# Optimization experiments

Measured on AMD Instinct MI355X. Metric: run time of the kernel, lower is better.

The kernel has to match this reference:

```python
import jax, jax.numpy as jnp
import numpy as np

L = 8          # num_layers
H = 1024       # hidden_size
F = 4096       # features_per_layer
B, S = 2, 1024 # batch, seq_len
P = L * (L + 1) // 2  # number of (layer -> target_layer) decoders


def setup_inputs() -> dict:
    key = jax.random.key(0)
    k0, k1, k2, k3 = jax.random.split(key, 4)
    res = jax.random.normal(k0, (L, B, S, H), jnp.float32)          # residual stream per layer
    We = jax.random.normal(k1, (L, F, H), jnp.float32) / np.sqrt(H)  # stacked encoder weights
    be = jnp.zeros((L, F), jnp.float32)
    Wd = jax.random.normal(k2, (P, H, F), jnp.float32) / np.sqrt(F)  # flattened decoder weights, pair (l,t>=l)
    bd = jnp.zeros((P, H), jnp.float32)
    thresh = jnp.full((L,), 0.03, jnp.float32)                       # JumpReLU thresholds
    return {"res": res, "We": We, "be": be, "Wd": Wd, "bd": bd, "thresh": thresh}


def reference(res, We, be, Wd, bd, thresh):
    # Encoders + JumpReLU (eval-mode: x * (x > threshold)) for all layers at once
    preact = jnp.einsum('lbsh,lfh->lbsf', res, We) + be[:, None, None, :]
    feats = jnp.where(preact > thresh[:, None, None, None], preact, jnp.zeros((), preact.dtype))

    # Cross-layer decoders: layer l writes to all targets t >= l (grouped GEMM per source layer)
    recon = jnp.zeros_like(res)
    for l in range(L):
        start = l * L - l * (l - 1) // 2
        k = L - l
        Wl = Wd[start:start + k]           # [k, H, F]
        bl = bd[start:start + k]           # [k, H]
        out = jnp.einsum('bsf,khf->kbsh', feats[l], Wl) + bl[:, None, None, :]
        recon = recon.at[l:].add(out)
    return recon, feats
```

## Files before the change

### kernel.cpp

```cpp
#include <hip/hip_runtime.h>


#define MT 2048
#define HD 1024
#define FD 4096
#define LL 8

typedef __attribute__((ext_vector_type(8))) short short8;
typedef __attribute__((ext_vector_type(4))) float f32x4;
typedef __attribute__((ext_vector_type(4))) unsigned short ushort4v;

typedef const __attribute__((address_space(1))) void GV;
typedef __attribute__((address_space(3))) void LV;

__device__ __forceinline__ void gload16(const void* g, void* l) {
  __builtin_amdgcn_global_load_lds((GV*)g, (LV*)l, 16, 0, 0);
}

#define BAR()                                  \
  do {                                         \
    __builtin_amdgcn_sched_barrier(0);         \
    __builtin_amdgcn_s_barrier();              \
    __builtin_amdgcn_sched_barrier(0);         \
  } while (0)

__device__ __forceinline__ unsigned int f2bf1(float x) {
  unsigned u = __float_as_uint(x);
  return (u + 0x7FFFu + ((u >> 16) & 1u)) >> 16;
}

__device__ __forceinline__ void load_tile(const float* __restrict__ base, int ld,
                                          float4* r) {
  const int t = threadIdx.x;
#pragma unroll
  for (int i = 0; i < 8; ++i) {
    int idx = t + 256 * i;
    int row = idx >> 4;
    int c4  = idx & 15;
    r[i] = *(const float4*)(base + (size_t)row * ld + c4 * 4);
  }
}

__device__ __forceinline__ void write_tile(char* lds, const float4* r) {
  const int t = threadIdx.x;
#pragma unroll
  for (int i = 0; i < 8; ++i) {
    int idx = t + 256 * i;
    int row = idx >> 4;
    int c4  = idx & 15;
    int off = (row * 128 + c4 * 8) ^ ((row & 7) << 4);
    unsigned lo = f2bf1(r[i].x) | (f2bf1(r[i].y) << 16);
    unsigned hi = f2bf1(r[i].z) | (f2bf1(r[i].w) << 16);
    *(uint2*)(lds + off) = make_uint2(lo, hi);
  }
}

__device__ __forceinline__ void load_tile_bf(const unsigned short* __restrict__ base,
                                             int ld, short8* r) {
  const int t = threadIdx.x;
#pragma unroll
  for (int i = 0; i < 4; ++i) {
    int idx = t + 256 * i;
    int row = idx >> 3;
    int c8  = idx & 7;
    r[i] = *(const short8*)(base + (size_t)row * ld + c8 * 8);
  }
}

__device__ __forceinline__ void write_tile_bf(char* lds, const short8* r) {
  const int t = threadIdx.x;
#pragma unroll
  for (int i = 0; i < 4; ++i) {
    int idx = t + 256 * i;
    int row = idx >> 3;
    int c8  = idx & 7;
    int off = (row * 128 + c8 * 16) ^ ((row & 7) << 4);
    *(short8*)(lds + off) = r[i];
  }
}

__device__ __forceinline__ void compute_tile(const char* sA, const char* sB,
                                             f32x4 acc[4][4], int wr, int wc,
                                             int l16, int h16) {
#pragma unroll
  for (int ks = 0; ks < 2; ++ks) {
    short8 a[4], b[4];
#pragma unroll
    for (int i = 0; i < 4; ++i) {
      int row = wr * 64 + i * 16 + l16;
      a[i] = *(const short8*)(sA + ((row * 128 + ks * 64 + h16 * 16) ^ ((row & 7) << 4)));
    }
#pragma unroll
    for (int j = 0; j < 4; ++j) {
      int col = wc * 64 + j * 16 + l16;
      b[j] = *(const short8*)(sB + ((col * 128 + ks * 64 + h16 * 16) ^ ((col & 7) << 4)));
    }
#pragma unroll
    for (int i = 0; i < 4; ++i)
#pragma unroll
      for (int j = 0; j < 4; ++j)
        acc[i][j] = __builtin_amdgcn_mfma_f32_16x16x32_bf16(a[i], b[j], acc[i][j], 0, 0, 0);
  }
}

__global__ __launch_bounds__(256, 2) void enc_kernel(
    const float* __restrict__ res, const float* __restrict__ We,
    const float* __restrict__ be, const float* __restrict__ thresh,
    float* __restrict__ feats, unsigned short* __restrict__ feats_bf,
    const float* __restrict__ wd_src, unsigned short* __restrict__ wd_dst,
    int conv_z) {
  __shared__ char sA[128 * 64 * 2];
  __shared__ char sB[128 * 64 * 2];

  if ((int)blockIdx.z < conv_z) {
    size_t chunk = ((size_t)blockIdx.z * 16 + blockIdx.y) * 32 + blockIdx.x;
    size_t base = chunk * 36864 + threadIdx.x;
    const float4* src = (const float4*)wd_src;
#pragma unroll 4
    for (int i = 0; i < 144; ++i) {
      size_t k = base + (size_t)i * 256;
      float4 v = src[k];
      ushort4v o;
      o.x = (unsigned short)f2bf1(v.x);
      o.y = (unsigned short)f2bf1(v.y);
      o.z = (unsigned short)f2bf1(v.z);
      o.w = (unsigned short)f2bf1(v.w);
      *(ushort4v*)(wd_dst + k * 4) = o;
    }
    return;
  }

  const int l  = blockIdx.z - conv_z;
  const int m0 = blockIdx.y * 128;
  const int f0 = blockIdx.x * 128;

  const float* Abase = res + (size_t)l * MT * HD + (size_t)m0 * HD;
  const float* Bbase = We  + (size_t)l * FD * HD + (size_t)f0 * HD;

  const int t = threadIdx.x;
  const int lane = t & 63, wave = t >> 6;
  const int wr = wave >> 1, wc = wave & 1;
  const int l16 = lane & 15, h16 = lane >> 4;

  f32x4 acc[4][4];
#pragma unroll
  for (int i = 0; i < 4; ++i)
#pragma unroll
    for (int j = 0; j < 4; ++j) acc[i][j] = (f32x4){0.f, 0.f, 0.f, 0.f};

  float4 ra[8], rb[8];
  load_tile(Abase, HD, ra);
  load_tile(Bbase, HD, rb);

  const int NK = HD / 64;
  for (int kt = 0; kt < NK; ++kt) {
    write_tile(sA, ra);
    write_tile(sB, rb);
    __syncthreads();
    if (kt + 1 < NK) {
      load_tile(Abase + (kt + 1) * 64, HD, ra);
      load_tile(Bbase + (kt + 1) * 64, HD, rb);
    }
    compute_tile(sA, sB, acc, wr, wc, l16, h16);
    __syncthreads();
  }

  const float th = thresh[l];
#pragma unroll
  for (int j = 0; j < 4; ++j) {
    int col = f0 + wc * 64 + j * 16 + l16;
    float bev = be[(size_t)l * FD + col];
#pragma unroll
    for (int i = 0; i < 4; ++i) {
      int rbase = m0 + wr * 64 + i * 16 + h16 * 4;
#pragma unroll
      for (int q = 0; q < 4; ++q) {
        float v = acc[i][j][q] + bev;
        float g = (v > th) ? v : 0.f;
        size_t idx = ((size_t)l * MT + rbase + q) * FD + col;
        feats[idx] = g;
        if (feats_bf) feats_bf[idx] = (unsigned short)f2bf1(g);
      }
    }
  }
}

#define DEC_ABUF 32768
#define DEC_BUFSZ 49152
__global__ __launch_bounds__(512, 2) void dec8(
    const unsigned short* __restrict__ featsbf,
    const unsigned short* __restrict__ wdbf,
    const float* __restrict__ bd, float* __restrict__ recon) {
  __shared__ char lds[3 * DEC_BUFSZ];

  const int flat = (int)(blockIdx.x + 8 * blockIdx.y + 64 * blockIdx.z);
  const int nf = (flat & 7) * 32 + (flat >> 3);
  const int bx = nf & 7;
  const int by = (nf >> 3) & 7;
  const int z  = nf >> 6;

  const int m0 = by * 256;
  const int h0 = bx * 128;

  const int t = threadIdx.x;
  const int L = t & 63;
  const int w = t >> 6;
  const int wm = w >> 1, wn = w & 1;
  const int l16 = L & 15, h16 = L >> 4;

  const int rl   = (t >> 3) & 7;
  const int scol = (t & 7) ^ rl;
  const int rowl = t >> 3;
  const size_t laneA = (size_t)(m0 + rowl) * FD + scol * 8;
  const size_t laneB = (size_t)(h0 + rowl) * FD + scol * 8;

  const int s0 = h16 ^ (l16 & 7);

  for (int sub = 0; sub < 2; ++sub) {
    const int lp = sub ? z : 7 - z;
    const int NT = (lp + 1) * 64;

    f32x4 acc[4][4];
#pragma unroll
    for (int i = 0; i < 4; ++i)
#pragma unroll
      for (int j = 0; j < 4; ++j) acc[i][j] = (f32x4){0.f, 0.f, 0.f, 0.f};

    auto stage = [&](int bi, int tt) {
      int l = tt >> 6, kt = tt & 63;
      int p = l * LL - ((l * (l - 1)) >> 1) + (lp - l);
      const unsigned short* Ab = featsbf + (size_t)l * MT * FD + kt * 64 + laneA;
      const unsigned short* Bb = wdbf + (size_t)p * HD * FD + kt * 64 + laneB;
      char* dA = lds + bi * DEC_BUFSZ + t * 16;
      char* dB = dA + DEC_ABUF;
#pragma unroll
      for (int i = 0; i < 4; ++i)
        gload16(Ab + (size_t)i * 64 * FD, dA + i * 8192);
#pragma unroll
      for (int i = 0; i < 2; ++i)
        gload16(Bb + (size_t)i * 64 * FD, dB + i * 8192);
    };

    auto rfrag = [&](int bi, int ks, short8* a, short8* b) {
      const char* cA = lds + bi * DEC_BUFSZ;
      const char* cB = cA + DEC_ABUF;
      const int sl = (s0 ^ (ks << 2)) << 4;
#pragma unroll
      for (int i = 0; i < 4; ++i) {
        int row = wm * 64 + i * 16 + l16;
        a[i] = *(const short8*)(cA + row * 128 + sl);
      }
#pragma unroll
      for (int j = 0; j < 4; ++j) {
        int col = wn * 64 + j * 16 + l16;
        b[j] = *(const short8*)(cB + col * 128 + sl);
      }
    };

    auto cluster = [&](const short8* a, const short8* b) {
      __builtin_amdgcn_s_setprio(1);
#pragma unroll
      for (int i = 0; i < 4; ++i)
#pragma unroll
        for (int j = 0; j < 4; ++j)
          acc[i][j] = __builtin_amdgcn_mfma_f32_16x16x32_bf16(a[i], b[j], acc[i][j], 0, 0, 0);
      __builtin_amdgcn_s_setprio(0);
    };

    stage(0, 0);
    stage(1, 1);
    asm volatile("s_waitcnt vmcnt(6)" ::: "memory");
    BAR();

    short8 aC[4], bC[4], aN[4], bN[4];
    rfrag(0, 0, aC, bC);

    int rd = 0;
    for (int tt = 0; tt < NT; ++tt) {
      int st = rd + 2;
      if (st >= 3) st -= 3;
      if (tt + 2 < NT) stage(st, tt + 2);
      rfrag(rd, 1, aN, bN);
      cluster(aC, bC);
      if (tt + 2 < NT) {
        asm volatile("s_waitcnt vmcnt(6)" ::: "memory");
      } else if (tt + 1 < NT) {
        asm volatile("s_waitcnt vmcnt(0)" ::: "memory");
      }
      BAR();
      int nrd = (rd + 1 == 3) ? 0 : rd + 1;
      if (tt + 1 < NT) rfrag(nrd, 0, aC, bC);
      cluster(aN, bN);
      rd = nrd;
    }

#pragma unroll
    for (int j = 0; j < 4; ++j) {
      int col = h0 + wn * 64 + j * 16 + l16;
      float bsum = 0.f;
      for (int l = 0; l <= lp; ++l) {
        int p = l * LL - ((l * (l - 1)) >> 1) + (lp - l);
        bsum += bd[(size_t)p * HD + col];
      }
#pragma unroll
      for (int i = 0; i < 4; ++i) {
        int rbase = m0 + wm * 64 + i * 16 + h16 * 4;
#pragma unroll
        for (int q = 0; q < 4; ++q)
          recon[((size_t)lp * MT + rbase + q) * HD + col] = acc[i][j][q] + bsum;
      }
    }
  }
}

template <bool ABF16>
__global__ __launch_bounds__(256, 2) void dec_kernel(
    const float* __restrict__ feats_f32, const unsigned short* __restrict__ feats_bf,
    const float* __restrict__ Wd, const float* __restrict__ bd,
    float* __restrict__ recon) {
  __shared__ char sA[128 * 64 * 2];
  __shared__ char sB[128 * 64 * 2];

  const int lp = (LL - 1) - (int)blockIdx.z;
  const int m0 = blockIdx.y * 128;
  const int h0 = blockIdx.x * 128;

  const int t = threadIdx.x;
  const int lane = t & 63, wave = t >> 6;
  const int wr = wave >> 1, wc = wave & 1;
  const int l16 = lane & 15, h16 = lane >> 4;

  f32x4 acc[4][4];
#pragma unroll
  for (int i = 0; i < 4; ++i)
#pragma unroll
    for (int j = 0; j < 4; ++j) acc[i][j] = (f32x4){0.f, 0.f, 0.f, 0.f};

  const int nit = (lp + 1) * (FD / 64);

  auto Abf = [&](int it) -> const unsigned short* {
    int l = it >> 6, kt = it & 63;
    return feats_bf + ((size_t)l * MT + m0) * FD + kt * 64;
  };
  auto Af = [&](int it) -> const float* {
    int l = it >> 6, kt = it & 63;
    return feats_f32 + ((size_t)l * MT + m0) * FD + kt * 64;
  };
  auto Bb = [&](int it) -> const float* {
    int l = it >> 6, kt = it & 63;
    int p = l * LL - l * (l - 1) / 2 + (lp - l);
    return Wd + ((size_t)p * HD + h0) * FD + kt * 64;
  };

  short8 rab[4];
  float4 raf[8];
  float4 rb[8];
  if constexpr (ABF16) load_tile_bf(Abf(0), FD, rab); else load_tile(Af(0), FD, raf);
  load_tile(Bb(0), FD, rb);

  for (int it = 0; it < nit; ++it) {
    if constexpr (ABF16) write_tile_bf(sA, rab); else write_tile(sA, raf);
    write_tile(sB, rb);
    __syncthreads();
    if (it + 1 < nit) {
      if constexpr (ABF16) load_tile_bf(Abf(it + 1), FD, rab);
      else                 load_tile(Af(it + 1), FD, raf);
      load_tile(Bb(it + 1), FD, rb);
    }
    compute_tile(sA, sB, acc, wr, wc, l16, h16);
    __syncthreads();
  }

#pragma unroll
  for (int j = 0; j < 4; ++j) {
    int col = h0 + wc * 64 + j * 16 + l16;
    float bsum = 0.f;
    for (int l = 0; l <= lp; ++l) {
      int p = l * LL - l * (l - 1) / 2 + (lp - l);
      bsum += bd[(size_t)p * HD + col];
    }
#pragma unroll
    for (int i = 0; i < 4; ++i) {
      int rbase = m0 + wr * 64 + i * 16 + h16 * 4;
#pragma unroll
      for (int q = 0; q < 4; ++q) {
        recon[((size_t)lp * MT + rbase + q) * HD + col] = acc[i][j][q] + bsum;
      }
    }
  }
}

extern "C" void kernel_launch(void* const* d_in, const int* in_sizes, int n_in,
                              void* d_out, int out_size, void* d_ws, size_t ws_size,
                              hipStream_t stream) {
  const float* res    = (const float*)d_in[0];
  const float* We     = (const float*)d_in[1];
  const float* be     = (const float*)d_in[2];
  const float* Wd     = (const float*)d_in[3];
  const float* bd     = (const float*)d_in[4];
  const float* thresh = (const float*)d_in[5];

  float* recon = (float*)d_out;
  float* feats = recon + (size_t)LL * MT * HD;

  const size_t featsbf_bytes = (size_t)LL * MT * FD * sizeof(unsigned short);
  const size_t wdbf_bytes    = (size_t)36 * HD * FD * sizeof(unsigned short);
  const bool use_bf   = ws_size >= featsbf_bytes;
  const bool use_full = ws_size >= featsbf_bytes + wdbf_bytes;

  unsigned short* feats_bf = use_bf ? (unsigned short*)d_ws : nullptr;
  unsigned short* wd_bf    = (unsigned short*)((char*)d_ws + featsbf_bytes);

  if (use_full) {
    enc_kernel<<<dim3(FD / 128, MT / 128, LL + 2), dim3(256), 0, stream>>>(
        res, We, be, thresh, feats, feats_bf, Wd, wd_bf, 2);
    dec8<<<dim3(HD / 128, MT / 256, 4), dim3(512), 0, stream>>>(
        feats_bf, wd_bf, bd, recon);
  } else {
    enc_kernel<<<dim3(FD / 128, MT / 128, LL), dim3(256), 0, stream>>>(
        res, We, be, thresh, feats, feats_bf, nullptr, nullptr, 0);
    if (use_bf)
      dec_kernel<true><<<dim3(HD / 128, MT / 128, LL), dim3(256), 0, stream>>>(
          feats, feats_bf, Wd, bd, recon);
    else
      dec_kernel<false><<<dim3(HD / 128, MT / 128, LL), dim3(256), 0, stream>>>(
          feats, nullptr, Wd, bd, recon);
  }
}
```

Before: 1.055 ms.

## Pre-convert inputs to bf16 and use a triple-buffered 256x128 encoder kernel

Adds a separate conversion kernel that turns res, We and Wd into bf16 in the workspace up front. A new enc8 encoder then runs a 256x128 tile with 512 threads, direct global-to-LDS loads and a three-stage LDS pipeline, reusing the dec8 structure instead of converting fp32 on the fly. This targets the encoder's fp32 load and conversion overhead and its shallow pipelining. In exchange it needs more workspace and an extra full pass of memory traffic for the conversion, and the new path runs only when the workspace is large enough.

Measured after the change: 1.003 ms, median of 2. 1.05x faster.

```diff
diff --git a/kernel.cpp b/kernel.cpp
--- a/kernel.cpp
+++ b/kernel.cpp
@@ -101,6 +101,30 @@
       for (int j = 0; j < 4; ++j)
         acc[i][j] = __builtin_amdgcn_mfma_f32_16x16x32_bf16(a[i], b[j], acc[i][j], 0, 0, 0);
   }
+}
+
+__global__ __launch_bounds__(256) void conv_kernel(
+    const float* __restrict__ res, const float* __restrict__ We,
+    const float* __restrict__ Wd, unsigned short* __restrict__ res_bf,
+    unsigned short* __restrict__ we_bf, unsigned short* __restrict__ wd_bf) {
+  const size_t stride = (size_t)gridDim.x * 256;
+  const size_t i0 = (size_t)blockIdx.x * 256 + threadIdx.x;
+  auto cv = [&](const float* __restrict__ s, unsigned short* __restrict__ d,
+                size_t n4) {
+    const float4* s4 = (const float4*)s;
+    for (size_t k = i0; k < n4; k += stride) {
+      float4 v = s4[k];
+      ushort4v o;
+      o.x = (unsigned short)f2bf1(v.x);
+      o.y = (unsigned short)f2bf1(v.y);
+      o.z = (unsigned short)f2bf1(v.z);
+      o.w = (unsigned short)f2bf1(v.w);
+      *(ushort4v*)(d + k * 4) = o;
+    }
+  };
+  cv(res, res_bf, (size_t)LL * MT * HD / 4);
+  cv(We,  we_bf,  (size_t)LL * FD * HD / 4);
+  cv(Wd,  wd_bf,  (size_t)36 * HD * FD / 4);
 }
 
 __global__ __launch_bounds__(256, 2) void enc_kernel(
@@ -187,6 +211,131 @@
 
 #define DEC_ABUF 32768
 #define DEC_BUFSZ 49152
+__global__ __launch_bounds__(512, 2) void enc8(
+    const unsigned short* __restrict__ resbf,
+    const unsigned short* __restrict__ webf,
+    const float* __restrict__ be, const float* __restrict__ thresh,
+    float* __restrict__ feats, unsigned short* __restrict__ feats_bf) {
+  __shared__ char lds[3 * DEC_BUFSZ];
+
+  const int flat = (int)(blockIdx.x + 32 * blockIdx.y + 256 * blockIdx.z);
+  const int nf = (flat & 7) * 256 + (flat >> 3);
+  const int bx = nf & 31;
+  const int by = (nf >> 5) & 7;
+  const int l  = nf >> 8;
+
+  const int m0 = by * 256;
+  const int f0 = bx * 128;
+
+  const int t = threadIdx.x;
+  const int L = t & 63;
+  const int w = t >> 6;
+  const int wm = w >> 1, wn = w & 1;
+  const int l16 = L & 15, h16 = L >> 4;
+
+  const int rl   = (t >> 3) & 7;
+  const int scol = (t & 7) ^ rl;
+  const int rowl = t >> 3;
+  const unsigned short* Abase = resbf + (size_t)l * MT * HD;
+  const unsigned short* Bbase = webf + (size_t)l * FD * HD;
+  const size_t laneA = (size_t)(m0 + rowl) * HD + scol * 8;
+  const size_t laneB = (size_t)(f0 + rowl) * HD + scol * 8;
+
+  const int s0 = h16 ^ (l16 & 7);
+  const int NT = HD / 64;
+
+  f32x4 acc[4][4];
+#pragma unroll
+  for (int i = 0; i < 4; ++i)
+#pragma unroll
+    for (int j = 0; j < 4; ++j) acc[i][j] = (f32x4){0.f, 0.f, 0.f, 0.f};
+
+  auto stage = [&](int bi, int tt) {
+    const unsigned short* Ab = Abase + (size_t)tt * 64 + laneA;
+    const unsigned short* Bb = Bbase + (size_t)tt * 64 + laneB;
+    char* dA = lds + bi * DEC_BUFSZ + t * 16;
+    char* dB = dA + DEC_ABUF;
+#pragma unroll
+    for (int i = 0; i < 4; ++i)
+      gload16(Ab + (size_t)i * 64 * HD, dA + i * 8192);
+#pragma unroll
+    for (int i = 0; i < 2; ++i)
+      gload16(Bb + (size_t)i * 64 * HD, dB + i * 8192);
+  };
+
+  auto rfrag = [&](int bi, int ks, short8* a, short8* b) {
+    const char* cA = lds + bi * DEC_BUFSZ;
+    const char* cB = cA + DEC_ABUF;
+    const int sl = (s0 ^ (ks << 2)) << 4;
+#pragma unroll
+    for (int i = 0; i < 4; ++i) {
+      int row = wm * 64 + i * 16 + l16;
+      a[i] = *(const short8*)(cA + row * 128 + sl);
+    }
+#pragma unroll
+    for (int j = 0; j < 4; ++j) {
+      int col = wn * 64 + j * 16 + l16;
+      b[j] = *(const short8*)(cB + col * 128 + sl);
+    }
+  };
+
+  auto cluster = [&](const short8* a, const short8* b) {
+    __builtin_amdgcn_s_setprio(1);
+#pragma unroll
+    for (int i = 0; i < 4; ++i)
+#pragma unroll
+      for (int j = 0; j < 4; ++j)
+        acc[i][j] = __builtin_amdgcn_mfma_f32_16x16x32_bf16(a[i], b[j], acc[i][j], 0, 0, 0);
+    __builtin_amdgcn_s_setprio(0);
+  };
+
+  stage(0, 0);
+  stage(1, 1);
+  asm volatile("s_waitcnt vmcnt(6)" ::: "memory");
+  BAR();
+
+  short8 aC[4], bC[4], aN[4], bN[4];
+  rfrag(0, 0, aC, bC);
+
+  int rd = 0;
+  for (int tt = 0; tt < NT; ++tt) {
+    int st = rd + 2;
+    if (st >= 3) st -= 3;
+    if (tt + 2 < NT) stage(st, tt + 2);
+    rfrag(rd, 1, aN, bN);
+    cluster(aC, bC);
+    if (tt + 2 < NT) {
+      asm volatile("s_waitcnt vmcnt(6)" ::: "memory");
+    } else if (tt + 1 < NT) {
+      asm volatile("s_waitcnt vmcnt(0)" ::: "memory");
+    }
+    BAR();
+    int nrd = (rd + 1 == 3) ? 0 : rd + 1;
+    if (tt + 1 < NT) rfrag(nrd, 0, aC, bC);
+    cluster(aN, bN);
+    rd = nrd;
+  }
+
+  const float th = thresh[l];
+#pragma unroll
+  for (int j = 0; j < 4; ++j) {
+    int col = f0 + wn * 64 + j * 16 + l16;
+    float bev = be[(size_t)l * FD + col];
+#pragma unroll
+    for (int i = 0; i < 4; ++i) {
+      int rbase = m0 + wm * 64 + i * 16 + h16 * 4;
+#pragma unroll
+      for (int q = 0; q < 4; ++q) {
+        float v = acc[i][j][q] + bev;
+        float g = (v > th) ? v : 0.f;
+        size_t idx = ((size_t)l * MT + rbase + q) * FD + col;
+        feats[idx] = g;
+        feats_bf[idx] = (unsigned short)f2bf1(g);
+      }
+    }
+  }
+}
+
 __global__ __launch_bounds__(512, 2) void dec8(
     const unsigned short* __restrict__ featsbf,
     const unsigned short* __restrict__ wdbf,
@@ -403,27 +552,38 @@
   float* recon = (float*)d_out;
   float* feats = recon + (size_t)LL * MT * HD;
 
-  const size_t featsbf_bytes = (size_t)LL * MT * FD * sizeof(unsigned short);
-  const size_t wdbf_bytes    = (size_t)36 * HD * FD * sizeof(unsigned short);
-  const bool use_bf   = ws_size >= featsbf_bytes;
-  const bool use_full = ws_size >= featsbf_bytes + wdbf_bytes;
-
-  unsigned short* feats_bf = use_bf ? (unsigned short*)d_ws : nullptr;
-  unsigned short* wd_bf    = (unsigned short*)((char*)d_ws + featsbf_bytes);
-
-  if (use_full) {
-    enc_kernel<<<dim3(FD / 128, MT / 128, LL + 2), dim3(256), 0, stream>>>(
+  const size_t featsbf_b = (size_t)LL * MT * FD * 2;
+  const size_t wdbf_b    = (size_t)36 * HD * FD * 2;
+  const size_t resbf_b   = (size_t)LL * MT * HD * 2;
+  const size_t webf_b    = (size_t)LL * FD * HD * 2;
+
+  const bool use_bf   = ws_size >= featsbf_b;
+  const bool use_full = ws_size >= featsbf_b + wdbf_b;
+  const bool use_v3   = ws_size >= featsbf_b + wdbf_b + resbf_b + webf_b;
+
+  unsigned short* feats_bf = (unsigned short*)d_ws;
+  unsigned short* wd_bf    = (unsigned short*)((char*)d_ws + featsbf_b);
+  unsigned short* res_bf   = (unsigned short*)((char*)d_ws + featsbf_b + wdbf_b);
+  unsigned short* we_bf    = (unsigned short*)((char*)d_ws + featsbf_b + wdbf_b + resbf_b);
+
+  if (use_v3) {
+    conv_kernel<<<dim3(2048), dim3(256), 0, stream>>>(res, We, Wd, res_bf, we_bf, wd_bf);
+    enc8<<<dim3(32, 8, 8), dim3(512), 0, stream>>>(res_bf, we_bf, be, thresh,
+                                                   feats, feats_bf);
+    dec8<<<dim3(8, 8, 4), dim3(512), 0, stream>>>(feats_bf, wd_bf, bd, recon);
+  } else if (use_full) {
+    enc_kernel<<<dim3(32, 16, LL + 2), dim3(256), 0, stream>>>(
         res, We, be, thresh, feats, feats_bf, Wd, wd_bf, 2);
-    dec8<<<dim3(HD / 128, MT / 256, 4), dim3(512), 0, stream>>>(
-        feats_bf, wd_bf, bd, recon);
+    dec8<<<dim3(8, 8, 4), dim3(512), 0, stream>>>(feats_bf, wd_bf, bd, recon);
+  } else if (use_bf) {
+    enc_kernel<<<dim3(32, 16, LL), dim3(256), 0, stream>>>(
+        res, We, be, thresh, feats, feats_bf, nullptr, nullptr, 0);
+    dec_kernel<true><<<dim3(8, 16, LL), dim3(256), 0, stream>>>(
+        feats, feats_bf, Wd, bd, recon);
   } else {
-    enc_kernel<<<dim3(FD / 128, MT / 128, LL), dim3(256), 0, stream>>>(
-        res, We, be, thresh, feats, feats_bf, nullptr, nullptr, 0);
-    if (use_bf)
-      dec_kernel<true><<<dim3(HD / 128, MT / 128, LL), dim3(256), 0, stream>>>(
-          feats, feats_bf, Wd, bd, recon);
-    else
-      dec_kernel<false><<<dim3(HD / 128, MT / 128, LL), dim3(256), 0, stream>>>(
-          feats, nullptr, Wd, bd, recon);
-  }
-}
+    enc_kernel<<<dim3(32, 16, LL), dim3(256), 0, stream>>>(
+        res, We, be, thresh, feats, nullptr, nullptr, nullptr, 0);
+    dec_kernel<false><<<dim3(8, 16, LL), dim3(256), 0, stream>>>(
+        feats, nullptr, Wd, bd, recon);
+  }
+}
```
